# Performance work log

Hardware: AMD Instinct MI355X
Metric: run time of the kernel (lower is better)

## Reference

```python
import jax, jax.numpy as jnp
import numpy as np

B, NN, BBX, CLS, LAT = 8192, 64, 6, 16, 128
IN = LAT + NN + CLS  # 208
NT = B * NN          # total nodes in batched graph
NE = 4_194_304       # random edges (avg degree 8)


def setup_inputs() -> dict:
    key = jax.random.key(0)
    ks = jax.random.split(key, 16)
    p = lambda i, sh: (jax.random.normal(ks[i], sh, dtype=jnp.float32) * 0.05)
    return {
        "embedding": jax.random.normal(ks[0], (B, IN), dtype=jnp.float32),
        "E": jax.random.randint(ks[1], (2, NE), 0, NT, dtype=jnp.int32),
        "refine_iter": 2,
        "W1": p(2, (IN, 128)), "b1": p(3, (128,)),
        "W2": p(4, (128, 128)), "b2": p(5, (128,)),
        "Wbbx": p(6, (128, NN * BBX)), "bbbx": p(7, (NN * BBX,)),
        "Wlbl": p(8, (128, NN)), "blbl": p(9, (NN,)),
        "Wedge": p(10, (128, NN * NN)), "bedge": p(11, (NN * NN,)),
        "Wcls": p(12, (128, CLS)), "bcls": p(13, (CLS,)),
        "Wg": p(14, (BBX, BBX)), "bg": p(15, (BBX,)),
    }


def _gcn(h, src, dst, Wg, bg):
    # PyG GCNConv with add_self_loops=True, bias: D^-1/2 (A+I) D^-1/2 (h W) + b
    deg = jax.ops.segment_sum(jnp.ones(src.shape, h.dtype), dst, num_segments=NT)
    dinv = jax.lax.rsqrt(deg)  # deg >= 1 thanks to self-loops
    norm = dinv[src] * dinv[dst]
    m = h @ Wg  # [NT, BBX]
    out = jax.ops.segment_sum(m[src] * norm[:, None], dst, num_segments=NT)
    return out + bg


def reference(embedding, E, refine_iter, W1, b1, W2, b2, Wbbx, bbbx,
              Wlbl, blbl, Wedge, bedge, Wcls, bcls, Wg, bg):
    sig = jax.nn.sigmoid
    x = sig(embedding @ W1 + b1)
    x = sig(x @ W2 + b2)
    x = sig(x @ W2 + b2)  # dense2 applied twice (shared weights), as in source
    x_bbx = sig(x @ Wbbx + bbbx).reshape(B, NN, BBX)
    x_lbl = sig(x @ Wlbl + blbl).reshape(B, NN, 1)
    x_edge = sig(x @ Wedge + bedge).reshape(B, NN, NN)
    class_pred = jax.nn.softmax(x @ Wcls + bcls, axis=-1)

    loops = jnp.arange(NT, dtype=E.dtype)
    src = jnp.concatenate([E[0], loops])
    dst = jnp.concatenate([E[1], loops])

    x_bbx_refined = x_bbx
    for _ in range(int(refine_iter)):
        x_masked = x_bbx_refined * x_lbl  # labels=None -> mask with x_lbl
        flat = x_masked.reshape(NT, BBX)
        corr = jax.nn.sigmoid(_gcn(flat, src, dst, Wg, bg))
        # NOTE: source adds correction to the MASKED features (faithful)
        x_bbx_refined = (flat + corr).reshape(B, NN, BBX)
    return (x_bbx, x_lbl, x_edge, class_pred, x_bbx_refined)
```

## Files before the change

kernel.cpp:

```cpp
#include <hip/hip_runtime.h>
#include <hip/hip_bf16.h>
#include <math.h>

#define B_      8192
#define IN_     208
#define INP_    224
#define H_      128
#define NN_     64
#define BBX_    6
#define CLS_    16
#define NT_     (B_*NN_)
#define NE_     4194304
#define NB_     256
#define BSH_    11
#define CH_     4096
#define CAP_    18432
#define GB_     (NT_/256)

typedef __attribute__((ext_vector_type(8))) short short8v;
typedef __attribute__((ext_vector_type(4))) float f32x4;
typedef __attribute__((ext_vector_type(2))) float f32x2;

__device__ __forceinline__ float sigmoidf_(float v){ return 1.0f/(1.0f+__expf(-v)); }
__device__ __forceinline__ unsigned f2bf_(float f){
  unsigned u = __float_as_uint(f);
  return (u + 0x7FFFu + ((u >> 16) & 1u)) >> 16;
}

#if defined(__has_builtin)
# if __has_builtin(__builtin_amdgcn_cvt_pk_fp8_f32) && __has_builtin(__builtin_amdgcn_cvt_pk_f32_fp8)
#  define HW_FP8 1
# endif
#endif
#ifndef HW_FP8
# define HW_FP8 0
#endif

#if !HW_FP8
__device__ __forceinline__ unsigned enc1_(float v){
  unsigned u = __float_as_uint(v);
  unsigned s = (u >> 31) << 7;
  unsigned a = u & 0x7FFFFFFFu;
  unsigned r8;
  if (a < 0x3D000000u) {
    int q = (int)rintf(__uint_as_float(a) * 512.0f);
    r8 = (unsigned)q;
  } else {
    unsigned r = a + 0x7FFFFu + ((a >> 20) & 1u);
    int eb = (int)(r >> 23) - 120;
    r8 = (eb > 15) ? 0x7Eu : (unsigned)((eb << 3) | ((r >> 20) & 7u));
  }
  return s | r8;
}
__device__ __forceinline__ float dec1_(unsigned b){
  unsigned m = b & 7u, e = (b >> 3) & 0xFu;
  float mag = e ? __uint_as_float(((e + 120u) << 23) | (m << 20))
               : (float)m * 0.001953125f;
  return (b & 0x80u) ? -mag : mag;
}
#endif

__device__ __forceinline__ uint2 enc6_(const float mm[6]){
  uint2 o;
#if HW_FP8
  int w0 = __builtin_amdgcn_cvt_pk_fp8_f32(mm[0], mm[1], 0, false);
  w0     = __builtin_amdgcn_cvt_pk_fp8_f32(mm[2], mm[3], w0, true);
  int w1 = __builtin_amdgcn_cvt_pk_fp8_f32(mm[4], mm[5], 0, false);
  o.x = (unsigned)w0; o.y = (unsigned)w1;
#else
  o.x = enc1_(mm[0]) | (enc1_(mm[1])<<8) | (enc1_(mm[2])<<16) | (enc1_(mm[3])<<24);
  o.y = enc1_(mm[4]) | (enc1_(mm[5])<<8);
#endif
  return o;
}
__device__ __forceinline__ void dec6_(uint2 w, float v[6]){
#if HW_FP8
  f32x2 a = __builtin_amdgcn_cvt_pk_f32_fp8(w.x, false);
  f32x2 b = __builtin_amdgcn_cvt_pk_f32_fp8(w.x, true);
  f32x2 c = __builtin_amdgcn_cvt_pk_f32_fp8(w.y, false);
  v[0]=a[0]; v[1]=a[1]; v[2]=b[0]; v[3]=b[1]; v[4]=c[0]; v[5]=c[1];
#else
  v[0]=dec1_(w.x & 255u); v[1]=dec1_((w.x>>8)&255u);
  v[2]=dec1_((w.x>>16)&255u); v[3]=dec1_(w.x>>24);
  v[4]=dec1_(w.y & 255u); v[5]=dec1_((w.y>>8)&255u);
#endif
}

__global__ __launch_bounds__(256) void binprep_k(
    const int* __restrict__ E, int* __restrict__ gcnt, unsigned* __restrict__ binned,
    const float* __restrict__ We, unsigned short* __restrict__ WtE,
    const float* __restrict__ Wb, unsigned short* __restrict__ WtB,
    const float* __restrict__ W2, unsigned short* __restrict__ Wt2,
    const float* __restrict__ Wl, unsigned short* __restrict__ WtL,
    const float* __restrict__ W1, unsigned short* __restrict__ W1t,
    const float* __restrict__ Wc, unsigned short* __restrict__ WtC)
{
  __shared__ char smem[23552];
  const int t = threadIdx.x;

  if (blockIdx.x >= 1024) {
    const int pb = blockIdx.x - 1024;
    if (pb >= 73) {
      const int i = (pb - 73) * 256 + t;
      if (i < H_ * INP_) {
        const int n = i / INP_, k = i % INP_;
        W1t[i] = (k < IN_) ? (unsigned short)f2bf_(W1[(size_t)k * H_ + n]) : 0;
      } else if (i < H_ * INP_ + CLS_ * H_) {
        const int j = i - H_ * INP_;
        const int n = j >> 7, k = j & 127;
        WtC[j] = (unsigned short)f2bf_(Wc[(size_t)k * CLS_ + n]);
      }
      return;
    }
    unsigned short (*tile)[136] = (unsigned short(*)[136])smem;
    const float* W; unsigned short* Wt; int N, n0;
    if (pb < 64)      { W = We; Wt = WtE; N = 4096; n0 = pb * 64; }
    else if (pb < 70) { W = Wb; Wt = WtB; N = 384;  n0 = (pb-64) * 64; }
    else if (pb < 72) { W = W2; Wt = Wt2; N = 128;  n0 = (pb-70) * 64; }
    else              { W = Wl; Wt = WtL; N = 64;   n0 = 0; }
    const int kk = t >> 6, nn = t & 63;
    for (int k0 = 0; k0 < 128; k0 += 4)
      tile[nn][k0 + kk] = (unsigned short)f2bf_(W[(size_t)(k0 + kk) * N + n0 + nn]);
    __syncthreads();
    const int rr = t >> 2, c0 = (t & 3) * 32;
    ushort4* dst = reinterpret_cast<ushort4*>(Wt + (size_t)(n0 + rr) * 128 + c0);
    #pragma unroll
    for (int q = 0; q < 8; ++q) {
      ushort4 o;
      o.x = tile[rr][c0 + q*4 + 0]; o.y = tile[rr][c0 + q*4 + 1];
      o.z = tile[rr][c0 + q*4 + 2]; o.w = tile[rr][c0 + q*4 + 3];
      dst[q] = o;
    }
    return;
  }

  unsigned* stage = (unsigned*)smem;
  unsigned char* stb = (unsigned char*)(smem + 16384);
  int* hist  = (int*)(smem + 20480);
  int* lbase = (int*)(smem + 21504);
  int* gbase = (int*)(smem + 22528);
  const int e0 = blockIdx.x * CH_;

  hist[t] = 0;
  __syncthreads();

  unsigned pk[CH_/256];
  int rb[CH_/256];
  #pragma unroll
  for (int i = 0; i < CH_/256; ++i) {
    const int e = e0 + i * 256 + t;
    const int s = E[e];
    const unsigned d = (unsigned)E[NE_ + e];
    const int b = d >> BSH_;
    pk[i] = (unsigned)s | ((d & 2047u) << 19);
    rb[i] = atomicAdd(&hist[b], 1) | (b << 20);
  }
  __syncthreads();

  const int v = hist[t];
  lbase[t] = v; __syncthreads();
  #pragma unroll
  for (int off = 1; off < NB_; off <<= 1) {
    int x = (t >= off) ? lbase[t - off] : 0;
    __syncthreads();
    lbase[t] += x;
    __syncthreads();
  }
  const int excl = lbase[t] - v;
  __syncthreads();
  lbase[t] = excl;
  gbase[t] = t * CAP_ + atomicAdd(&gcnt[t], v);
  __syncthreads();

  #pragma unroll
  for (int i = 0; i < CH_/256; ++i) {
    const int b = rb[i] >> 20;
    const int pos = lbase[b] + (rb[i] & 0xFFFFF);
    stage[pos] = pk[i];
    stb[pos] = (unsigned char)b;
  }
  __syncthreads();

  for (int i = t; i < CH_; i += 256) {
    const int b = stb[i];
    const int tgt = gbase[b] + (i - lbase[b]);
    if (tgt < (b + 1) * CAP_)
      binned[tgt] = stage[i];
  }
}

__global__ __launch_bounds__(1024) void csr_k(const int* __restrict__ gcnt,
                                              const unsigned* __restrict__ binned,
                                              int2* __restrict__ rowcnt,
                                              float* __restrict__ dinv, int* __restrict__ csr_src) {
  __shared__ int cnt[2048];
  __shared__ int sd[1024];
  const int t = threadIdx.x, b = blockIdx.x;
  const int beg = b * CAP_;
  const int end = beg + min(gcnt[b], CAP_);

  cnt[t] = 0; cnt[t + 1024] = 0;
  __syncthreads();
  for (int i = beg + t; i < end; i += 1024)
    atomicAdd(&cnt[binned[i] >> 19], 1);
  __syncthreads();

  const int c0 = cnt[2 * t], c1 = cnt[2 * t + 1];
  const int s = c0 + c1;
  sd[t] = s; __syncthreads();
  #pragma unroll
  for (int off = 1; off < 1024; off <<= 1) {
    int x = (t >= off) ? sd[t - off] : 0;
    __syncthreads();
    sd[t] += x;
    __syncthreads();
  }
  const int excl = sd[t] - s;

  const int node0 = b * 2048 + 2 * t;
  rowcnt[node0]     = make_int2(beg + excl, c0);
  rowcnt[node0 + 1] = make_int2(beg + excl + c0, c1);
  dinv[node0]       = rsqrtf(1.0f + (float)c0);
  dinv[node0 + 1]   = rsqrtf(1.0f + (float)c1);
  __syncthreads();
  cnt[2 * t] = excl;
  cnt[2 * t + 1] = excl + c0;
  __syncthreads();

  for (int i = beg + t; i < end; i += 1024) {
    const unsigned pk = binned[i];
    const int dl = pk >> 19;
    const int slot = atomicAdd(&cnt[dl], 1);
    csr_src[beg + slot] = (int)(pk & 0x7FFFFu);
  }
}

__global__ __launch_bounds__(256) void fused_trunk_k(
    const float* __restrict__ emb,
    const unsigned short* __restrict__ W1t,
    const float* __restrict__ b1,
    const unsigned short* __restrict__ W2t,
    const float* __restrict__ b2,
    const unsigned short* __restrict__ WtL,
    const float* __restrict__ blbl,
    const unsigned short* __restrict__ WtC,
    const float* __restrict__ bcls,
    unsigned short* __restrict__ Xb,
    float* __restrict__ o_lbl, float* __restrict__ o_cls)
{
  __shared__ unsigned short s[64][136];
  const int tid  = threadIdx.x;
  const int wave = tid >> 6, lane = tid & 63;
  const int wm = wave >> 1, wn = wave & 1;
  const int r = lane & 15, g = lane >> 4;
  const int colB0 = wn * 64;
  const int grow0 = blockIdx.x * 64;

  f32x4 acc[2][4];
  short8v a[2], b[4];

  #pragma unroll
  for (int i = 0; i < 2; ++i)
    #pragma unroll
    for (int j = 0; j < 4; ++j)
      acc[i][j] = (f32x4){0.f, 0.f, 0.f, 0.f};

  for (int ks = 0; ks < INP_/32; ++ks) {
    const int koff = ks * 32 + g * 8;
    #pragma unroll
    for (int i = 0; i < 2; ++i) {
      if (koff < IN_) {
        const float* src = emb + (size_t)(grow0 + wm*32 + i*16 + r) * IN_ + koff;
        float4 v0 = *reinterpret_cast<const float4*>(src);
        float4 v1 = *reinterpret_cast<const float4*>(src + 4);
        a[i][0]=(short)f2bf_(v0.x); a[i][1]=(short)f2bf_(v0.y);
        a[i][2]=(short)f2bf_(v0.z); a[i][3]=(short)f2bf_(v0.w);
        a[i][4]=(short)f2bf_(v1.x); a[i][5]=(short)f2bf_(v1.y);
        a[i][6]=(short)f2bf_(v1.z); a[i][7]=(short)f2bf_(v1.w);
      } else {
        a[i] = (short8v){0,0,0,0,0,0,0,0};
      }
    }
    #pragma unroll
    for (int j = 0; j < 4; ++j)
      b[j] = *reinterpret_cast<const short8v*>(W1t + (size_t)(colB0 + j*16 + r) * INP_ + koff);
    #pragma unroll
    for (int i = 0; i < 2; ++i)
      #pragma unroll
      for (int j = 0; j < 4; ++j)
        acc[i][j] = __builtin_amdgcn_mfma_f32_16x16x32_bf16(a[i], b[j], acc[i][j], 0, 0, 0);
  }
  #pragma unroll
  for (int j = 0; j < 4; ++j) {
    const int col = colB0 + j*16 + r;
    const float bc = b1[col];
    #pragma unroll
    for (int i = 0; i < 2; ++i)
      #pragma unroll
      for (int q = 0; q < 4; ++q)
        s[wm*32 + i*16 + g*4 + q][col] = (unsigned short)f2bf_(sigmoidf_(acc[i][j][q] + bc));
  }
  __syncthreads();

  for (int layer = 0; layer < 2; ++layer) {
    #pragma unroll
    for (int i = 0; i < 2; ++i)
      #pragma unroll
      for (int j = 0; j < 4; ++j)
        acc[i][j] = (f32x4){0.f, 0.f, 0.f, 0.f};

    #pragma unroll
    for (int ks = 0; ks < 4; ++ks) {
      const int koff = ks * 32 + g * 8;
      #pragma unroll
      for (int i = 0; i < 2; ++i)
        a[i] = *reinterpret_cast<const short8v*>(&s[wm*32 + i*16 + r][koff]);
      #pragma unroll
      for (int j = 0; j < 4; ++j)
        b[j] = *reinterpret_cast<const short8v*>(W2t + (size_t)(colB0 + j*16 + r) * H_ + koff);
      #pragma unroll
      for (int i = 0; i < 2; ++i)
        #pragma unroll
        for (int j = 0; j < 4; ++j)
          acc[i][j] = __builtin_amdgcn_mfma_f32_16x16x32_bf16(a[i], b[j], acc[i][j], 0, 0, 0);
    }
    __syncthreads();

    #pragma unroll
    for (int j = 0; j < 4; ++j) {
      const int col = colB0 + j*16 + r;
      const float bc = b2[col];
      #pragma unroll
      for (int i = 0; i < 2; ++i) {
        #pragma unroll
        for (int q = 0; q < 4; ++q) {
          const float v = sigmoidf_(acc[i][j][q] + bc);
          const unsigned short vb = (unsigned short)f2bf_(v);
          s[wm*32 + i*16 + g*4 + q][col] = vb;
          if (layer == 1)
            Xb[(size_t)(grow0 + wm*32 + i*16 + g*4 + q) * H_ + col] = vb;
        }
      }
    }
    __syncthreads();
  }

  {
    f32x4 accl[4];
    #pragma unroll
    for (int j = 0; j < 4; ++j) accl[j] = (f32x4){0.f, 0.f, 0.f, 0.f};
    #pragma unroll
    for (int ks = 0; ks < 4; ++ks) {
      const int koff = ks * 32 + g * 8;
      const short8v av = *reinterpret_cast<const short8v*>(&s[wave*16 + r][koff]);
      #pragma unroll
      for (int j = 0; j < 4; ++j) {
        const short8v bv = *reinterpret_cast<const short8v*>(WtL + (size_t)(j*16 + r) * H_ + koff);
        accl[j] = __builtin_amdgcn_mfma_f32_16x16x32_bf16(av, bv, accl[j], 0, 0, 0);
      }
    }
    #pragma unroll
    for (int j = 0; j < 4; ++j) {
      const int col = j*16 + r;
      const float bc = blbl[col];
      #pragma unroll
      for (int q = 0; q < 4; ++q) {
        const int row = grow0 + wave*16 + g*4 + q;
        o_lbl[(size_t)row * NN_ + col] = sigmoidf_(accl[j][q] + bc);
      }
    }
  }

  {
    f32x4 accc = (f32x4){0.f, 0.f, 0.f, 0.f};
    #pragma unroll
    for (int ks = 0; ks < 4; ++ks) {
      const int koff = ks * 32 + g * 8;
      const short8v av = *reinterpret_cast<const short8v*>(&s[wave*16 + r][koff]);
      const short8v bv = *reinterpret_cast<const short8v*>(WtC + (size_t)r * H_ + koff);
      accc = __builtin_amdgcn_mfma_f32_16x16x32_bf16(av, bv, accc, 0, 0, 0);
    }
    const float bc = bcls[r];
    #pragma unroll
    for (int q = 0; q < 4; ++q) {
      float v = accc[q] + bc;
      float mx = v;
      for (int off = 8; off; off >>= 1) mx = fmaxf(mx, __shfl_xor(mx, off, 16));
      const float e = __expf(v - mx);
      float sm = e;
      for (int off = 8; off; off >>= 1) sm += __shfl_xor(sm, off, 16);
      const int row = grow0 + wave*16 + g*4 + q;
      o_cls[(size_t)row * CLS_ + r] = e / sm;
    }
  }
}

__global__ __launch_bounds__(256) void gemm_mfma_head(
    const unsigned short* __restrict__ Xb,
    const unsigned short* __restrict__ Wt,
    const float* __restrict__ bias, float* __restrict__ C, int N)
{
  const int tid  = threadIdx.x;
  const int wave = tid >> 6, lane = tid & 63;
  const int wm = wave >> 1, wn = wave & 1;
  const int r = lane & 15, g = lane >> 4;
  const int rowA0 = blockIdx.y * 128 + wm * 64;
  const int colB0 = blockIdx.x * 128 + wn * 64;

  f32x4 acc[4][4];
  #pragma unroll
  for (int i = 0; i < 4; ++i)
    #pragma unroll
    for (int j = 0; j < 4; ++j)
      acc[i][j] = (f32x4){0.f, 0.f, 0.f, 0.f};

  #pragma unroll
  for (int ks = 0; ks < 4; ++ks) {
    const int koff = ks * 32 + g * 8;
    short8v a[4], b[4];
    #pragma unroll
    for (int i = 0; i < 4; ++i)
      a[i] = *reinterpret_cast<const short8v*>(Xb + (size_t)(rowA0 + i*16 + r) * 128 + koff);
    #pragma unroll
    for (int j = 0; j < 4; ++j)
      b[j] = *reinterpret_cast<const short8v*>(Wt + (size_t)(colB0 + j*16 + r) * 128 + koff);
    #pragma unroll
    for (int i = 0; i < 4; ++i)
      #pragma unroll
      for (int j = 0; j < 4; ++j)
        acc[i][j] = __builtin_amdgcn_mfma_f32_16x16x32_bf16(a[i], b[j], acc[i][j], 0, 0, 0);
  }

  #pragma unroll
  for (int j = 0; j < 4; ++j) {
    const int col = colB0 + j*16 + r;
    const float bc = bias[col];
    #pragma unroll
    for (int i = 0; i < 4; ++i) {
      const int row0 = rowA0 + i*16 + g*4;
      #pragma unroll
      for (int q = 0; q < 4; ++q)
        C[(size_t)(row0 + q) * N + col] = sigmoidf_(acc[i][j][q] + bc);
    }
  }
}

__global__ __launch_bounds__(256) void gcn_pre_k(
    const float* __restrict__ refined, const float* __restrict__ lbl,
    const float* __restrict__ Wg, const float* __restrict__ dinv,
    uint2* __restrict__ ms8)
{
  int i = blockIdx.x * 256 + threadIdx.x;
  if (i >= NT_) return;
  float l = lbl[i];
  float di = dinv[i];
  float f[6];
  #pragma unroll
  for (int j = 0; j < 6; ++j) f[j] = refined[(size_t)i * 6 + j] * l;
  float mm[6];
  #pragma unroll
  for (int j = 0; j < 6; ++j) {
    float acc = 0.f;
    #pragma unroll
    for (int k = 0; k < 6; ++k) acc = fmaf(f[k], Wg[k * 6 + j], acc);
    mm[j] = acc * di;
  }
  ms8[i] = enc6_(mm);
}

template<int WRITE_MS>
__device__ __forceinline__ void gather_body(
    int i,
    const float* __restrict__ rin, float* __restrict__ rout,
    const float* __restrict__ lbl,
    const uint2* __restrict__ ms8_in, uint2* __restrict__ ms8_out,
    const float* __restrict__ dinv,
    const int2* __restrict__ rowcnt, const int* __restrict__ csr_src,
    const float* __restrict__ bg, const float* __restrict__ Wg)
{
  const float di = dinv[i];
  const float l  = lbl[i];
  const int2 rc = rowcnt[i];
  const int beg = rc.x;
  const int kend = beg + rc.y;

  float acc[6];
  dec6_(ms8_in[i], acc);

  int k = beg;
  for (; k + 3 < kend; k += 4) {
    const int s0 = csr_src[k],   s1 = csr_src[k+1];
    const int s2 = csr_src[k+2], s3 = csr_src[k+3];
    const uint2 w0 = ms8_in[s0], w1 = ms8_in[s1];
    const uint2 w2 = ms8_in[s2], w3 = ms8_in[s3];
    float v0[6], v1[6], v2[6], v3[6];
    dec6_(w0, v0); dec6_(w1, v1); dec6_(w2, v2); dec6_(w3, v3);
    #pragma unroll
    for (int j = 0; j < 6; ++j) acc[j] += (v0[j] + v1[j]) + (v2[j] + v3[j]);
  }
  for (; k < kend; ++k) {
    float v[6];
    dec6_(ms8_in[csr_src[k]], v);
    #pragma unroll
    for (int j = 0; j < 6; ++j) acc[j] += v[j];
  }

  float nr[6];
  #pragma unroll
  for (int j = 0; j < 6; ++j) {
    const float flat = rin[(size_t)i * 6 + j] * l;
    nr[j] = flat + sigmoidf_(di * acc[j] + bg[j]);
    rout[(size_t)i * 6 + j] = nr[j];
  }

  if (WRITE_MS) {
    float f[6], mm[6];
    #pragma unroll
    for (int j = 0; j < 6; ++j) f[j] = nr[j] * l;
    #pragma unroll
    for (int j = 0; j < 6; ++j) {
      float a = 0.f;
      #pragma unroll
      for (int kk = 0; kk < 6; ++kk) a = fmaf(f[kk], Wg[kk * 6 + j], a);
      mm[j] = a * di;
    }
    ms8_out[i] = enc6_(mm);
  }
}

__global__ __launch_bounds__(256) void gcn_gather1_k(
    const float* __restrict__ rin, float* __restrict__ rout,
    const float* __restrict__ lbl,
    const uint2* __restrict__ ms8_in, uint2* __restrict__ ms8_out,
    const float* __restrict__ dinv,
    const int2* __restrict__ rowcnt, const int* __restrict__ csr_src,
    const float* __restrict__ bg, const float* __restrict__ Wg)
{
  const int i = blockIdx.x * 256 + threadIdx.x;
  gather_body<1>(i, rin, rout, lbl, ms8_in, ms8_out, dinv, rowcnt, csr_src, bg, Wg);
}

__global__ __launch_bounds__(256) void tail_k(
    float* __restrict__ o_ref, const float* __restrict__ lbl,
    const uint2* __restrict__ ms8_in,
    const float* __restrict__ dinv,
    const int2* __restrict__ rowcnt, const int* __restrict__ csr_src,
    const float* __restrict__ bg, const float* __restrict__ Wg,
    const unsigned short* __restrict__ Xb, const unsigned short* __restrict__ WtE,
    const float* __restrict__ bedge, float* __restrict__ o_edge)
{
  if (blockIdx.x < GB_) {
    const int i = blockIdx.x * 256 + threadIdx.x;
    gather_body<0>(i, o_ref, o_ref, lbl, ms8_in, nullptr, dinv, rowcnt, csr_src, bg, Wg);
    return;
  }
  const int bx = blockIdx.x - GB_;
  const int tm = bx >> 6;
  const int tn = bx & 63;
  const int tid  = threadIdx.x;
  const int wave = tid >> 6, lane = tid & 63;
  const int wm = wave >> 1, wn = wave & 1;
  const int r = lane & 15, g = lane >> 4;
  const int row0 = tm * 64 + wm * 32;
  const int col0 = tn * 64 + wn * 32;

  f32x4 acc[2][2];
  #pragma unroll
  for (int i = 0; i < 2; ++i)
    #pragma unroll
    for (int j = 0; j < 2; ++j)
      acc[i][j] = (f32x4){0.f, 0.f, 0.f, 0.f};

  #pragma unroll
  for (int ks = 0; ks < 4; ++ks) {
    const int koff = ks * 32 + g * 8;
    short8v a[2], b[2];
    #pragma unroll
    for (int i = 0; i < 2; ++i)
      a[i] = *reinterpret_cast<const short8v*>(Xb + (size_t)(row0 + i*16 + r) * 128 + koff);
    #pragma unroll
    for (int j = 0; j < 2; ++j)
      b[j] = *reinterpret_cast<const short8v*>(WtE + (size_t)(col0 + j*16 + r) * 128 + koff);
    #pragma unroll
    for (int i = 0; i < 2; ++i)
      #pragma unroll
      for (int j = 0; j < 2; ++j)
        acc[i][j] = __builtin_amdgcn_mfma_f32_16x16x32_bf16(a[i], b[j], acc[i][j], 0, 0, 0);
  }

  #pragma unroll
  for (int j = 0; j < 2; ++j) {
    const int col = col0 + j*16 + r;
    const float bc = bedge[col];
    #pragma unroll
    for (int i = 0; i < 2; ++i) {
      const int rr0 = row0 + i*16 + g*4;
      #pragma unroll
      for (int q = 0; q < 4; ++q)
        o_edge[(size_t)(rr0 + q) * 4096 + col] = sigmoidf_(acc[i][j][q] + bc);
    }
  }
}

extern "C" void kernel_launch(void* const* d_in, const int* in_sizes, int n_in,
                              void* d_out, int out_size, void* d_ws, size_t ws_size,
                              hipStream_t stream)
{
  const float* emb   = (const float*)d_in[0];
  const int*   E     = (const int*)  d_in[1];
  const float* W1    = (const float*)d_in[3];
  const float* b1    = (const float*)d_in[4];
  const float* W2    = (const float*)d_in[5];
  const float* b2    = (const float*)d_in[6];
  const float* Wbbx  = (const float*)d_in[7];
  const float* bbbx  = (const float*)d_in[8];
  const float* Wlbl  = (const float*)d_in[9];
  const float* blbl  = (const float*)d_in[10];
  const float* Wedge = (const float*)d_in[11];
  const float* bedge = (const float*)d_in[12];
  const float* Wcls  = (const float*)d_in[13];
  const float* bcls  = (const float*)d_in[14];
  const float* Wg    = (const float*)d_in[15];
  const float* bg    = (const float*)d_in[16];

  float* out    = (float*)d_out;
  float* o_bbx  = out;
  float* o_lbl  = out + 3145728;
  float* o_edge = out + 3670016;
  float* o_cls  = out + 37224448;
  float* o_ref  = out + 37355520;

  char* wsb = (char*)d_ws;
  unsigned short* WtL  = (unsigned short*)wsb;
  unsigned short* WtC  = WtL + (size_t)NN_ * H_;
  unsigned short* W1t  = WtC + (size_t)CLS_ * H_;
  unsigned short* W2t  = W1t + (size_t)H_ * INP_;
  unsigned short* Wt_e = W2t + (size_t)H_ * H_;
  unsigned short* Wt_b = Wt_e + (size_t)4096 * H_;
  unsigned short* Xb   = Wt_b + (size_t)384 * H_;
  float* dinv    = (float*)(Xb + (size_t)B_ * H_);
  int2*  rowcnt  = (int2*)(dinv + NT_);
  int*   csr_src = (int*)(rowcnt + NT_);
  char*  U       = (char*)(csr_src + (size_t)NB_ * CAP_);
  unsigned* binned = (unsigned*)U;
  uint2* ms8A    = (uint2*)U;
  uint2* ms8B    = ms8A + NT_;
  int*   gcnt    = (int*)(U + (size_t)NB_ * CAP_ * 4);

  hipMemsetAsync(gcnt, 0, NB_ * sizeof(int), stream);
  binprep_k<<<1024 + 73 + (H_*INP_ + CLS_*H_ + 255)/256, 256, 0, stream>>>(
      E, gcnt, binned,
      Wedge, Wt_e, Wbbx, Wt_b, W2, W2t, Wlbl, WtL, W1, W1t, Wcls, WtC);
  csr_k<<<NB_, 1024, 0, stream>>>(gcnt, binned, rowcnt, dinv, csr_src);
  fused_trunk_k<<<B_/64, 256, 0, stream>>>(emb, W1t, b1, W2t, b2,
                                           WtL, blbl, WtC, bcls, Xb, o_lbl, o_cls);
  gemm_mfma_head<<<dim3(384/128, B_/128), 256, 0, stream>>>(Xb, Wt_b, bbbx, o_bbx, 384);
  gcn_pre_k<<<NT_/256, 256, 0, stream>>>(o_bbx, o_lbl, Wg, dinv, ms8A);
  gcn_gather1_k<<<GB_, 256, 0, stream>>>(o_bbx, o_ref, o_lbl, ms8A, ms8B,
                                         dinv, rowcnt, csr_src, bg, Wg);
  tail_k<<<GB_ + 8192, 256, 0, stream>>>(o_ref, o_lbl, ms8B, dinv, rowcnt, csr_src,
                                         bg, Wg, Xb, Wt_e, bedge, o_edge);
}
```

Measured before the change: 240.1 us.

## Split edge GEMM out of tail kernel and unroll gather by eight

Removes the combined tail kernel that overlapped the second GCN gather with the edge-head MFMA GEMM. The edge head now runs as its own launch through the generic gemm_mfma_head, and the second gather becomes a separate templated kernel launch. The gather loop gains an 8-way unrolled path that issues eight index loads and then eight gathers, to expose more memory-level parallelism. This gives up the overlap of gather and GEMM in one grid and adds a launch, and the generic GEMM path may differ in efficiency for the 4096-column output.

```diff
diff --git a/kernel.cpp b/kernel.cpp
--- a/kernel.cpp
+++ b/kernel.cpp
@@ -469,66 +469,7 @@
 }
 
 template<int WRITE_MS>
-__device__ __forceinline__ void gather_body(
-    int i,
-    const float* __restrict__ rin, float* __restrict__ rout,
-    const float* __restrict__ lbl,
-    const uint2* __restrict__ ms8_in, uint2* __restrict__ ms8_out,
-    const float* __restrict__ dinv,
-    const int2* __restrict__ rowcnt, const int* __restrict__ csr_src,
-    const float* __restrict__ bg, const float* __restrict__ Wg)
-{
-  const float di = dinv[i];
-  const float l  = lbl[i];
-  const int2 rc = rowcnt[i];
-  const int beg = rc.x;
-  const int kend = beg + rc.y;
-
-  float acc[6];
-  dec6_(ms8_in[i], acc);
-
-  int k = beg;
-  for (; k + 3 < kend; k += 4) {
-    const int s0 = csr_src[k],   s1 = csr_src[k+1];
-    const int s2 = csr_src[k+2], s3 = csr_src[k+3];
-    const uint2 w0 = ms8_in[s0], w1 = ms8_in[s1];
-    const uint2 w2 = ms8_in[s2], w3 = ms8_in[s3];
-    float v0[6], v1[6], v2[6], v3[6];
-    dec6_(w0, v0); dec6_(w1, v1); dec6_(w2, v2); dec6_(w3, v3);
-    #pragma unroll
-    for (int j = 0; j < 6; ++j) acc[j] += (v0[j] + v1[j]) + (v2[j] + v3[j]);
-  }
-  for (; k < kend; ++k) {
-    float v[6];
-    dec6_(ms8_in[csr_src[k]], v);
-    #pragma unroll
-    for (int j = 0; j < 6; ++j) acc[j] += v[j];
-  }
-
-  float nr[6];
-  #pragma unroll
-  for (int j = 0; j < 6; ++j) {
-    const float flat = rin[(size_t)i * 6 + j] * l;
-    nr[j] = flat + sigmoidf_(di * acc[j] + bg[j]);
-    rout[(size_t)i * 6 + j] = nr[j];
-  }
-
-  if (WRITE_MS) {
-    float f[6], mm[6];
-    #pragma unroll
-    for (int j = 0; j < 6; ++j) f[j] = nr[j] * l;
-    #pragma unroll
-    for (int j = 0; j < 6; ++j) {
-      float a = 0.f;
-      #pragma unroll
-      for (int kk = 0; kk < 6; ++kk) a = fmaf(f[kk], Wg[kk * 6 + j], a);
-      mm[j] = a * di;
-    }
-    ms8_out[i] = enc6_(mm);
-  }
-}
-
-__global__ __launch_bounds__(256) void gcn_gather1_k(
+__global__ __launch_bounds__(256) void gcn_gather_k(
     const float* __restrict__ rin, float* __restrict__ rout,
     const float* __restrict__ lbl,
     const uint2* __restrict__ ms8_in, uint2* __restrict__ ms8_out,
@@ -537,68 +478,68 @@
     const float* __restrict__ bg, const float* __restrict__ Wg)
 {
   const int i = blockIdx.x * 256 + threadIdx.x;
-  gather_body<1>(i, rin, rout, lbl, ms8_in, ms8_out, dinv, rowcnt, csr_src, bg, Wg);
-}
-
-__global__ __launch_bounds__(256) void tail_k(
-    float* __restrict__ o_ref, const float* __restrict__ lbl,
-    const uint2* __restrict__ ms8_in,
-    const float* __restrict__ dinv,
-    const int2* __restrict__ rowcnt, const int* __restrict__ csr_src,
-    const float* __restrict__ bg, const float* __restrict__ Wg,
-    const unsigned short* __restrict__ Xb, const unsigned short* __restrict__ WtE,
-    const float* __restrict__ bedge, float* __restrict__ o_edge)
-{
-  if (blockIdx.x < GB_) {
-    const int i = blockIdx.x * 256 + threadIdx.x;
-    gather_body<0>(i, o_ref, o_ref, lbl, ms8_in, nullptr, dinv, rowcnt, csr_src, bg, Wg);
-    return;
-  }
-  const int bx = blockIdx.x - GB_;
-  const int tm = bx >> 6;
-  const int tn = bx & 63;
-  const int tid  = threadIdx.x;
-  const int wave = tid >> 6, lane = tid & 63;
-  const int wm = wave >> 1, wn = wave & 1;
-  const int r = lane & 15, g = lane >> 4;
-  const int row0 = tm * 64 + wm * 32;
-  const int col0 = tn * 64 + wn * 32;
-
-  f32x4 acc[2][2];
-  #pragma unroll
-  for (int i = 0; i < 2; ++i)
-    #pragma unroll
-    for (int j = 0; j < 2; ++j)
-      acc[i][j] = (f32x4){0.f, 0.f, 0.f, 0.f};
-
-  #pragma unroll
-  for (int ks = 0; ks < 4; ++ks) {
-    const int koff = ks * 32 + g * 8;
-    short8v a[2], b[2];
-    #pragma unroll
-    for (int i = 0; i < 2; ++i)
-      a[i] = *reinterpret_cast<const short8v*>(Xb + (size_t)(row0 + i*16 + r) * 128 + koff);
-    #pragma unroll
-    for (int j = 0; j < 2; ++j)
-      b[j] = *reinterpret_cast<const short8v*>(WtE + (size_t)(col0 + j*16 + r) * 128 + koff);
-    #pragma unroll
-    for (int i = 0; i < 2; ++i)
-      #pragma unroll
-      for (int j = 0; j < 2; ++j)
-        acc[i][j] = __builtin_amdgcn_mfma_f32_16x16x32_bf16(a[i], b[j], acc[i][j], 0, 0, 0);
-  }
-
-  #pragma unroll
-  for (int j = 0; j < 2; ++j) {
-    const int col = col0 + j*16 + r;
-    const float bc = bedge[col];
-    #pragma unroll
-    for (int i = 0; i < 2; ++i) {
-      const int rr0 = row0 + i*16 + g*4;
-      #pragma unroll
-      for (int q = 0; q < 4; ++q)
-        o_edge[(size_t)(rr0 + q) * 4096 + col] = sigmoidf_(acc[i][j][q] + bc);
-    }
+  const float di = dinv[i];
+  const float l  = lbl[i];
+  const int2 rc = rowcnt[i];
+  const int beg = rc.x;
+  const int kend = beg + rc.y;
+
+  float acc[6];
+  dec6_(ms8_in[i], acc);
+
+  int k = beg;
+  for (; k + 7 < kend; k += 8) {
+    int s_[8];
+    uint2 w_[8];
+    #pragma unroll
+    for (int u = 0; u < 8; ++u) s_[u] = csr_src[k + u];
+    #pragma unroll
+    for (int u = 0; u < 8; ++u) w_[u] = ms8_in[s_[u]];
+    #pragma unroll
+    for (int u = 0; u < 8; ++u) {
+      float v[6];
+      dec6_(w_[u], v);
+      #pragma unroll
+      for (int j = 0; j < 6; ++j) acc[j] += v[j];
+    }
+  }
+  for (; k + 3 < kend; k += 4) {
+    const int s0 = csr_src[k],   s1 = csr_src[k+1];
+    const int s2 = csr_src[k+2], s3 = csr_src[k+3];
+    const uint2 w0 = ms8_in[s0], w1 = ms8_in[s1];
+    const uint2 w2 = ms8_in[s2], w3 = ms8_in[s3];
+    float v0[6], v1[6], v2[6], v3[6];
+    dec6_(w0, v0); dec6_(w1, v1); dec6_(w2, v2); dec6_(w3, v3);
+    #pragma unroll
+    for (int j = 0; j < 6; ++j) acc[j] += (v0[j] + v1[j]) + (v2[j] + v3[j]);
+  }
+  for (; k < kend; ++k) {
+    float v[6];
+    dec6_(ms8_in[csr_src[k]], v);
+    #pragma unroll
+    for (int j = 0; j < 6; ++j) acc[j] += v[j];
+  }
+
+  float nr[6];
+  #pragma unroll
+  for (int j = 0; j < 6; ++j) {
+    const float flat = rin[(size_t)i * 6 + j] * l;
+    nr[j] = flat + sigmoidf_(di * acc[j] + bg[j]);
+    rout[(size_t)i * 6 + j] = nr[j];
+  }
+
+  if (WRITE_MS) {
+    float f[6], mm[6];
+    #pragma unroll
+    for (int j = 0; j < 6; ++j) f[j] = nr[j] * l;
+    #pragma unroll
+    for (int j = 0; j < 6; ++j) {
+      float a = 0.f;
+      #pragma unroll
+      for (int kk = 0; kk < 6; ++kk) a = fmaf(f[kk], Wg[kk * 6 + j], a);
+      mm[j] = a * di;
+    }
+    ms8_out[i] = enc6_(mm);
   }
 }
 
@@ -654,10 +595,11 @@
   csr_k<<<NB_, 1024, 0, stream>>>(gcnt, binned, rowcnt, dinv, csr_src);
   fused_trunk_k<<<B_/64, 256, 0, stream>>>(emb, W1t, b1, W2t, b2,
                                            WtL, blbl, WtC, bcls, Xb, o_lbl, o_cls);
-  gemm_mfma_head<<<dim3(384/128, B_/128), 256, 0, stream>>>(Xb, Wt_b, bbbx, o_bbx, 384);
+  gemm_mfma_head<<<dim3(4096/128, B_/128), 256, 0, stream>>>(Xb, Wt_e, bedge, o_edge, 4096);
+  gemm_mfma_head<<<dim3(384/128,  B_/128), 256, 0, stream>>>(Xb, Wt_b, bbbx,  o_bbx,  384);
   gcn_pre_k<<<NT_/256, 256, 0, stream>>>(o_bbx, o_lbl, Wg, dinv, ms8A);
-  gcn_gather1_k<<<GB_, 256, 0, stream>>>(o_bbx, o_ref, o_lbl, ms8A, ms8B,
-                                         dinv, rowcnt, csr_src, bg, Wg);
-  tail_k<<<GB_ + 8192, 256, 0, stream>>>(o_ref, o_lbl, ms8B, dinv, rowcnt, csr_src,
-                                         bg, Wg, Xb, Wt_e, bedge, o_edge);
-}
+  gcn_gather_k<1><<<GB_, 256, 0, stream>>>(o_bbx, o_ref, o_lbl, ms8A, ms8B,
+                                           dinv, rowcnt, csr_src, bg, Wg);
+  gcn_gather_k<0><<<GB_, 256, 0, stream>>>(o_ref, o_ref, o_lbl, ms8B, nullptr,
+                                           dinv, rowcnt, csr_src, bg, Wg);
+}
```

Measured after the change: 216.7 us, median of 2. 1.11x faster.
